# Performance work log

Hardware: AMD Instinct MI355X
Metric: run time of the kernel (lower is better)

The kernel has to match this reference:

```python
import jax, jax.numpy as jnp
import numpy as np

PATCH = 9  # patch_size (search window 9x9, i.e. displacement radius 4)


def setup_inputs() -> dict:
    key = jax.random.key(0)
    k1, k2 = jax.random.split(key)
    input1 = jax.random.normal(k1, (8, 128, 96, 128), dtype=jnp.float32)
    input2 = jax.random.normal(k2, (8, 128, 96, 128), dtype=jnp.float32)
    return {"input1": input1, "input2": input2}


def _correlation(input1, input2):
    # kernel_size=1, stride=1, padding=0, dilation=1, dilation_patch=1
    b, c, h, w = input1.shape
    pad_lo = (PATCH - 1) // 2
    pad_hi = PATCH // 2
    p2 = jnp.pad(input2, ((0, 0), (0, 0), (pad_lo, pad_hi), (pad_lo, pad_hi)))

    offs = jnp.arange(PATCH)
    ii, jj = jnp.meshgrid(offs, offs, indexing="ij")
    shifts = jnp.stack([ii.ravel(), jj.ravel()], axis=-1)  # (PATCH*PATCH, 2)

    def one_shift(off):
        win = jax.lax.dynamic_slice(p2, (0, 0, off[0], off[1]), (b, c, h, w))
        # channel-wise dot product at every spatial location
        return jnp.einsum("bchw,bchw->bhw", input1, win)

    corr = jax.vmap(one_shift)(shifts)          # (PATCH*PATCH, b, h, w)
    corr = corr.reshape(PATCH, PATCH, b, h, w)
    return corr.transpose(2, 0, 1, 3, 4)        # (b, PATCH, PATCH, h, w)


def reference(input1, input2):
    return _correlation(input1, input2)
```

## Files before the change

### kernel.cpp

```cpp
#include <hip/hip_runtime.h>

#define HH 96
#define WW 128
#define PP 9
#define RAD 4
#define YT 2
#define CCH 8
#define NCHUNK 16
#define TDI 3
#define ROWS2 (YT + TDI - 1)
#define GS 137
#define NG2 (ROWS2 * 136)
#define NT 384
#define PX 2
#define CHS (HH * WW)

typedef __fp16 h2v __attribute__((ext_vector_type(2)));
union HU { unsigned int u; h2v h; };

__device__ __forceinline__ unsigned int pk(float a, float b) {
    HU r; r.h = __builtin_amdgcn_cvt_pkrtz(a, b); return r.u;
}
__device__ __forceinline__ float dot2(unsigned int a, unsigned int b, float c) {
    HU ua, ub; ua.u = a; ub.u = b;
    return __builtin_amdgcn_fdot2(ua.h, ub.h, c, false);
}
__device__ __forceinline__ int swz(int g) { return g ^ ((g >> 3) & 7); }

__global__ __launch_bounds__(NT, 6)
void corr_kernel(const float* __restrict__ in1, const float* __restrict__ in2,
                 float* __restrict__ out)
{
    __shared__ uint4 s2[2][ROWS2 * GS];
    __shared__ uint4 s1[2][YT * GS];

    const int tid = threadIdx.x;
    const int y0  = blockIdx.x * YT;
    const int b   = blockIdx.y;
    const int dib = blockIdx.z * TDI;

    const int yl  = tid / (TDI * 64);
    const int rem = tid - yl * (TDI * 64);
    const int di3 = rem >> 6;
    const int xg  = rem & 63;
    const int x0  = xg * PX;

    const float* b1 = in1 + (size_t)b * 128 * CHS;
    const float* b2 = in2 + (size_t)b * 128 * CHS;

    const int r0  = tid / 136;
    const int l0  = tid - r0 * 136;
    const int gy0 = y0 - RAD + dib + r0;
    const int gx0 = l0 - RAD;
    const bool v0 = ((unsigned)gy0 < HH) && ((unsigned)gx0 < WW);
    const float* p0 = b2 + (gy0 * WW + gx0);
    const int d0  = r0 * GS + swz(l0);

    const int s1i   = tid + NT;
    const bool k1in2 = (s1i < NG2);
    const int r1a = s1i / 136;
    const int l1a = s1i - r1a * 136;
    const int gy1 = y0 - RAD + dib + r1a;
    const int gx1 = l1a - RAD;
    const int t1  = s1i - NG2;
    const int r1b = t1 >> 7;
    const int x1b = t1 & 127;
    const bool v1 = k1in2 ? (((unsigned)gy1 < HH) && ((unsigned)gx1 < WW)) : true;
    const float* p1 = k1in2 ? (b2 + (gy1 * WW + gx1))
                            : (b1 + ((y0 + r1b) * WW + x1b));
    const int d1  = k1in2 ? (r1a * GS + swz(l1a)) : (r1b * GS + swz(x1b));

    const bool act2 = (tid < 32);
    const float* p2 = b1 + ((y0 + 1) * WW + (96 + tid));
    const int d2  = GS + swz(96 + tid);

    float acc[PP][PX];
    #pragma unroll
    for (int j = 0; j < PP; ++j) { acc[j][0] = 0.f; acc[j][1] = 0.f; }

    for (int cc = 0; cc < NCHUNK; ++cc) {
        const int buf = cc & 1;
        const int co  = cc * CCH * CHS;

        {
            float f[8];
            #pragma unroll
            for (int j = 0; j < 8; ++j) f[j] = v0 ? p0[co + j * CHS] : 0.f;
            uint4 g;
            g.x = pk(f[0], f[1]); g.y = pk(f[2], f[3]);
            g.z = pk(f[4], f[5]); g.w = pk(f[6], f[7]);
            s2[buf][d0] = g;
        }
        {
            float f[8];
            #pragma unroll
            for (int j = 0; j < 8; ++j) f[j] = v1 ? p1[co + j * CHS] : 0.f;
            uint4 g;
            g.x = pk(f[0], f[1]); g.y = pk(f[2], f[3]);
            g.z = pk(f[4], f[5]); g.w = pk(f[6], f[7]);
            if (k1in2) s2[buf][d1] = g; else s1[buf][d1] = g;
        }
        if (act2) {
            float f[8];
            #pragma unroll
            for (int j = 0; j < 8; ++j) f[j] = p2[co + j * CHS];
            uint4 g;
            g.x = pk(f[0], f[1]); g.y = pk(f[2], f[3]);
            g.z = pk(f[4], f[5]); g.w = pk(f[6], f[7]);
            s1[buf][d2] = g;
        }
        __syncthreads();

        {
            const uint4* ar = &s1[buf][yl * GS];
            const uint4 a0 = ar[swz(x0)];
            const uint4 a1 = ar[swz(x0 + 1)];
            const uint4* r2 = &s2[buf][(yl + di3) * GS];
            #pragma unroll
            for (int w = 0; w < PX + PP - 1; ++w) {
                const uint4 v = r2[swz(x0 + w)];
                if (w <= PP - 1) {
                    float t = acc[w][0];
                    t = dot2(v.x, a0.x, t); t = dot2(v.y, a0.y, t);
                    t = dot2(v.z, a0.z, t); t = dot2(v.w, a0.w, t);
                    acc[w][0] = t;
                }
                if (w >= 1) {
                    float t = acc[w - 1][1];
                    t = dot2(v.x, a1.x, t); t = dot2(v.y, a1.y, t);
                    t = dot2(v.z, a1.z, t); t = dot2(v.w, a1.w, t);
                    acc[w - 1][1] = t;
                }
            }
        }
    }

    const int y  = y0 + yl;
    const int di = dib + di3;
    #pragma unroll
    for (int dj = 0; dj < PP; ++dj) {
        float* op = out + ((((size_t)(b * PP + di)) * PP + dj) * HH + y) * WW + x0;
        *reinterpret_cast<float2*>(op) = make_float2(acc[dj][0], acc[dj][1]);
    }
}

extern "C" void kernel_launch(void* const* d_in, const int* in_sizes, int n_in,
                              void* d_out, int out_size, void* d_ws, size_t ws_size,
                              hipStream_t stream) {
    const float* in1 = (const float*)d_in[0];
    const float* in2 = (const float*)d_in[1];
    float* out = (float*)d_out;
    dim3 grid(HH / YT, 8, 3);
    dim3 block(NT);
    corr_kernel<<<grid, block, 0, stream>>>(in1, in2, out);
}
```

Measured before the change: 164.8 us.

## Software-pipeline global loads of next channel chunk behind LDS compute

Prefetches the next channel chunk from global memory into registers before computing on the current LDS buffer, then packs and stores it into the other LDS buffer after compute. This puts a single barrier per iteration and overlaps global-load latency with dot-product work. The occupancy hint in launch bounds drops from 6 to 4 waves-per-EU groups to leave room for the extra prefetch registers, which lowers the latency hiding available from occupancy.

```diff
diff --git a/kernel.cpp b/kernel.cpp
--- a/kernel.cpp
+++ b/kernel.cpp
@@ -14,6 +14,7 @@
 #define NT 384
 #define PX 2
 #define CHS (HH * WW)
+#define CSTEP (CCH * CHS)
 
 typedef __fp16 h2v __attribute__((ext_vector_type(2)));
 union HU { unsigned int u; h2v h; };
@@ -27,7 +28,7 @@
 }
 __device__ __forceinline__ int swz(int g) { return g ^ ((g >> 3) & 7); }
 
-__global__ __launch_bounds__(NT, 6)
+__global__ __launch_bounds__(NT, 4)
 void corr_kernel(const float* __restrict__ in1, const float* __restrict__ in2,
                  float* __restrict__ out)
 {
@@ -78,38 +79,47 @@
     #pragma unroll
     for (int j = 0; j < PP; ++j) { acc[j][0] = 0.f; acc[j][1] = 0.f; }
 
+    float f0[8], f1[8], f2[8];
+
+    #pragma unroll
+    for (int j = 0; j < 8; ++j) f0[j] = v0 ? p0[j * CHS] : 0.f;
+    #pragma unroll
+    for (int j = 0; j < 8; ++j) f1[j] = v1 ? p1[j * CHS] : 0.f;
+    if (act2) {
+        #pragma unroll
+        for (int j = 0; j < 8; ++j) f2[j] = p2[j * CHS];
+    }
+    {
+        uint4 g;
+        g.x = pk(f0[0], f0[1]); g.y = pk(f0[2], f0[3]);
+        g.z = pk(f0[4], f0[5]); g.w = pk(f0[6], f0[7]);
+        s2[0][d0] = g;
+        g.x = pk(f1[0], f1[1]); g.y = pk(f1[2], f1[3]);
+        g.z = pk(f1[4], f1[5]); g.w = pk(f1[6], f1[7]);
+        if (k1in2) s2[0][d1] = g; else s1[0][d1] = g;
+        if (act2) {
+            g.x = pk(f2[0], f2[1]); g.y = pk(f2[2], f2[3]);
+            g.z = pk(f2[4], f2[5]); g.w = pk(f2[6], f2[7]);
+            s1[0][d2] = g;
+        }
+    }
+    __syncthreads();
+
     for (int cc = 0; cc < NCHUNK; ++cc) {
         const int buf = cc & 1;
-        const int co  = cc * CCH * CHS;
+        const bool more = (cc + 1 < NCHUNK);
+        const int co = (cc + 1) * CSTEP;
 
-        {
-            float f[8];
+        if (more) {
             #pragma unroll
-            for (int j = 0; j < 8; ++j) f[j] = v0 ? p0[co + j * CHS] : 0.f;
-            uint4 g;
-            g.x = pk(f[0], f[1]); g.y = pk(f[2], f[3]);
-            g.z = pk(f[4], f[5]); g.w = pk(f[6], f[7]);
-            s2[buf][d0] = g;
+            for (int j = 0; j < 8; ++j) f0[j] = v0 ? p0[co + j * CHS] : 0.f;
+            #pragma unroll
+            for (int j = 0; j < 8; ++j) f1[j] = v1 ? p1[co + j * CHS] : 0.f;
+            if (act2) {
+                #pragma unroll
+                for (int j = 0; j < 8; ++j) f2[j] = p2[co + j * CHS];
+            }
         }
-        {
-            float f[8];
-            #pragma unroll
-            for (int j = 0; j < 8; ++j) f[j] = v1 ? p1[co + j * CHS] : 0.f;
-            uint4 g;
-            g.x = pk(f[0], f[1]); g.y = pk(f[2], f[3]);
-            g.z = pk(f[4], f[5]); g.w = pk(f[6], f[7]);
-            if (k1in2) s2[buf][d1] = g; else s1[buf][d1] = g;
-        }
-        if (act2) {
-            float f[8];
-            #pragma unroll
-            for (int j = 0; j < 8; ++j) f[j] = p2[co + j * CHS];
-            uint4 g;
-            g.x = pk(f[0], f[1]); g.y = pk(f[2], f[3]);
-            g.z = pk(f[4], f[5]); g.w = pk(f[6], f[7]);
-            s1[buf][d2] = g;
-        }
-        __syncthreads();
 
         {
             const uint4* ar = &s1[buf][yl * GS];
@@ -133,6 +143,22 @@
                 }
             }
         }
+
+        if (more) {
+            uint4 g;
+            g.x = pk(f0[0], f0[1]); g.y = pk(f0[2], f0[3]);
+            g.z = pk(f0[4], f0[5]); g.w = pk(f0[6], f0[7]);
+            s2[buf ^ 1][d0] = g;
+            g.x = pk(f1[0], f1[1]); g.y = pk(f1[2], f1[3]);
+            g.z = pk(f1[4], f1[5]); g.w = pk(f1[6], f1[7]);
+            if (k1in2) s2[buf ^ 1][d1] = g; else s1[buf ^ 1][d1] = g;
+            if (act2) {
+                g.x = pk(f2[0], f2[1]); g.y = pk(f2[2], f2[3]);
+                g.z = pk(f2[4], f2[5]); g.w = pk(f2[6], f2[7]);
+                s1[buf ^ 1][d2] = g;
+            }
+        }
+        __syncthreads();
     }
 
     const int y  = y0 + yl;
```

New measurement: 182.1 us. 1.1x slower.

## Split width into two 64-column tiles and load float2 pairs per thread

Applied to the files above, without the earlier changes.

Each block now covers half the image width (64 columns plus an 8-column halo) with 192 threads, and the grid doubles along x. Staging loads fetch float2 pairs so each thread packs two LDS entries per chunk, which cuts the number of global load instructions. This raises block count and occupancy flexibility. The cost is extra halo reloads of input2 (72 of 64 columns per tile) and unchanged launch bounds, which were tuned for the larger block.

```diff
diff --git a/kernel.cpp b/kernel.cpp
--- a/kernel.cpp
+++ b/kernel.cpp
@@ -9,11 +9,15 @@
 #define NCHUNK 16
 #define TDI 3
 #define ROWS2 (YT + TDI - 1)
-#define GS 137
-#define NG2 (ROWS2 * 136)
-#define NT 384
-#define PX 2
+#define WB 64
+#define HALO (WB + 2 * RAD)
+#define GS2 73
+#define GS1 65
+#define NPAIR2 (ROWS2 * (HALO / 2))
+#define NPAIR1 (YT * (WB / 2))
+#define NT 192
 #define CHS (HH * WW)
+#define CSTEP (CCH * CHS)
 
 typedef __fp16 h2v __attribute__((ext_vector_type(2)));
 union HU { unsigned int u; h2v h; };
@@ -31,94 +35,95 @@
 void corr_kernel(const float* __restrict__ in1, const float* __restrict__ in2,
                  float* __restrict__ out)
 {
-    __shared__ uint4 s2[2][ROWS2 * GS];
-    __shared__ uint4 s1[2][YT * GS];
+    __shared__ uint4 s2[2][ROWS2 * GS2];
+    __shared__ uint4 s1[2][YT * GS1];
 
     const int tid = threadIdx.x;
-    const int y0  = blockIdx.x * YT;
+    const int by  = blockIdx.x >> 1;
+    const int bx  = blockIdx.x & 1;
+    const int y0  = by * YT;
+    const int x0b = bx * WB;
     const int b   = blockIdx.y;
     const int dib = blockIdx.z * TDI;
 
-    const int yl  = tid / (TDI * 64);
-    const int rem = tid - yl * (TDI * 64);
-    const int di3 = rem >> 6;
-    const int xg  = rem & 63;
-    const int x0  = xg * PX;
+    const int di3 = tid >> 6;
+    const int yl  = (tid >> 5) & 1;
+    const int xg  = tid & 31;
+    const int x0l = 2 * xg;
 
     const float* b1 = in1 + (size_t)b * 128 * CHS;
     const float* b2 = in2 + (size_t)b * 128 * CHS;
 
-    const int r0  = tid / 136;
-    const int l0  = tid - r0 * 136;
-    const int gy0 = y0 - RAD + dib + r0;
-    const int gx0 = l0 - RAD;
-    const bool v0 = ((unsigned)gy0 < HH) && ((unsigned)gx0 < WW);
-    const float* p0 = b2 + (gy0 * WW + gx0);
-    const int d0  = r0 * GS + swz(l0);
+    const float* tp0; int dA0, dB0; bool tv0, t0is2;
+    if (tid < NPAIR2) {
+        const int row = tid / 36;
+        const int pp  = tid - row * 36;
+        const int gy  = y0 - RAD + dib + row;
+        const int gx  = x0b + 2 * pp - RAD;
+        t0is2 = true;
+        tv0   = ((unsigned)gy < HH) && ((unsigned)gx < WW);
+        tp0   = b2 + (gy * WW + gx);
+        dA0   = row * GS2 + swz(2 * pp);
+        dB0   = row * GS2 + swz(2 * pp + 1);
+    } else {
+        const int u   = tid - NPAIR2;
+        const int row = u >> 5;
+        const int pp  = u & 31;
+        t0is2 = false;
+        tv0   = true;
+        tp0   = b1 + ((y0 + row) * WW + x0b + 2 * pp);
+        dA0   = row * GS1 + swz(2 * pp);
+        dB0   = row * GS1 + swz(2 * pp + 1);
+    }
+    const bool act1 = (tid < 16);
+    const float* tp1 = b1 + ((y0 + 1) * WW + x0b + 2 * (16 + tid));
+    const int dA1 = GS1 + swz(2 * (16 + tid));
+    const int dB1 = GS1 + swz(2 * (16 + tid) + 1);
 
-    const int s1i   = tid + NT;
-    const bool k1in2 = (s1i < NG2);
-    const int r1a = s1i / 136;
-    const int l1a = s1i - r1a * 136;
-    const int gy1 = y0 - RAD + dib + r1a;
-    const int gx1 = l1a - RAD;
-    const int t1  = s1i - NG2;
-    const int r1b = t1 >> 7;
-    const int x1b = t1 & 127;
-    const bool v1 = k1in2 ? (((unsigned)gy1 < HH) && ((unsigned)gx1 < WW)) : true;
-    const float* p1 = k1in2 ? (b2 + (gy1 * WW + gx1))
-                            : (b1 + ((y0 + r1b) * WW + x1b));
-    const int d1  = k1in2 ? (r1a * GS + swz(l1a)) : (r1b * GS + swz(x1b));
-
-    const bool act2 = (tid < 32);
-    const float* p2 = b1 + ((y0 + 1) * WW + (96 + tid));
-    const int d2  = GS + swz(96 + tid);
-
-    float acc[PP][PX];
+    float acc[PP][2];
     #pragma unroll
     for (int j = 0; j < PP; ++j) { acc[j][0] = 0.f; acc[j][1] = 0.f; }
 
     for (int cc = 0; cc < NCHUNK; ++cc) {
         const int buf = cc & 1;
-        const int co  = cc * CCH * CHS;
+        const int co  = cc * CSTEP;
 
         {
-            float f[8];
+            float2 f[8];
             #pragma unroll
-            for (int j = 0; j < 8; ++j) f[j] = v0 ? p0[co + j * CHS] : 0.f;
-            uint4 g;
-            g.x = pk(f[0], f[1]); g.y = pk(f[2], f[3]);
-            g.z = pk(f[4], f[5]); g.w = pk(f[6], f[7]);
-            s2[buf][d0] = g;
+            for (int j = 0; j < 8; ++j)
+                f[j] = tv0 ? *reinterpret_cast<const float2*>(tp0 + co + j * CHS)
+                           : make_float2(0.f, 0.f);
+            uint4 gA, gB;
+            gA.x = pk(f[0].x, f[1].x); gA.y = pk(f[2].x, f[3].x);
+            gA.z = pk(f[4].x, f[5].x); gA.w = pk(f[6].x, f[7].x);
+            gB.x = pk(f[0].y, f[1].y); gB.y = pk(f[2].y, f[3].y);
+            gB.z = pk(f[4].y, f[5].y); gB.w = pk(f[6].y, f[7].y);
+            if (t0is2) { s2[buf][dA0] = gA; s2[buf][dB0] = gB; }
+            else       { s1[buf][dA0] = gA; s1[buf][dB0] = gB; }
         }
-        {
-            float f[8];
+        if (act1) {
+            float2 f[8];
             #pragma unroll
-            for (int j = 0; j < 8; ++j) f[j] = v1 ? p1[co + j * CHS] : 0.f;
-            uint4 g;
-            g.x = pk(f[0], f[1]); g.y = pk(f[2], f[3]);
-            g.z = pk(f[4], f[5]); g.w = pk(f[6], f[7]);
-            if (k1in2) s2[buf][d1] = g; else s1[buf][d1] = g;
-        }
-        if (act2) {
-            float f[8];
-            #pragma unroll
-            for (int j = 0; j < 8; ++j) f[j] = p2[co + j * CHS];
-            uint4 g;
-            g.x = pk(f[0], f[1]); g.y = pk(f[2], f[3]);
-            g.z = pk(f[4], f[5]); g.w = pk(f[6], f[7]);
-            s1[buf][d2] = g;
+            for (int j = 0; j < 8; ++j)
+                f[j] = *reinterpret_cast<const float2*>(tp1 + co + j * CHS);
+            uint4 gA, gB;
+            gA.x = pk(f[0].x, f[1].x); gA.y = pk(f[2].x, f[3].x);
+            gA.z = pk(f[4].x, f[5].x); gA.w = pk(f[6].x, f[7].x);
+            gB.x = pk(f[0].y, f[1].y); gB.y = pk(f[2].y, f[3].y);
+            gB.z = pk(f[4].y, f[5].y); gB.w = pk(f[6].y, f[7].y);
+            s1[buf][dA1] = gA; s1[buf][dB1] = gB;
         }
         __syncthreads();
 
         {
-            const uint4* ar = &s1[buf][yl * GS];
-            const uint4 a0 = ar[swz(x0)];
-            const uint4 a1 = ar[swz(x0 + 1)];
-            const uint4* r2 = &s2[buf][(yl + di3) * GS];
+            const uint4* ar = &s1[buf][yl * GS1];
+            const uint4 a0 = ar[swz(x0l)];
+            const uint4 a1 = ar[swz(x0l + 1)];
+            const uint4* r2 = &s2[buf][(yl + di3) * GS2];
             #pragma unroll
-            for (int w = 0; w < PX + PP - 1; ++w) {
-                const uint4 v = r2[swz(x0 + w)];
+            for (int w = 0; w < PP + 1; ++w) {
+                const uint4 v = r2[swz(x0l + w)];
                 if (w <= PP - 1) {
                     float t = acc[w][0];
                     t = dot2(v.x, a0.x, t); t = dot2(v.y, a0.y, t);
@@ -137,9 +142,10 @@
 
     const int y  = y0 + yl;
     const int di = dib + di3;
+    const int xo = x0b + x0l;
     #pragma unroll
     for (int dj = 0; dj < PP; ++dj) {
-        float* op = out + ((((size_t)(b * PP + di)) * PP + dj) * HH + y) * WW + x0;
+        float* op = out + ((((size_t)(b * PP + di)) * PP + dj) * HH + y) * WW + xo;
         *reinterpret_cast<float2*>(op) = make_float2(acc[dj][0], acc[dj][1]);
     }
 }
@@ -150,7 +156,7 @@
     const float* in1 = (const float*)d_in[0];
     const float* in2 = (const float*)d_in[1];
     float* out = (float*)d_out;
-    dim3 grid(HH / YT, 8, 3);
+    dim3 grid((HH / YT) * 2, 8, 3);
     dim3 block(NT);
     corr_kernel<<<grid, block, 0, stream>>>(in1, in2, out);
 }
```

Measured after the change: 180.3 us. 9.4% more time.
